# Performance work log

Hardware: AMD Instinct MI355X
Metric: run time of the kernel (lower is better)

## Reference

```python
import jax, jax.numpy as jnp
import numpy as np

B, L = 256, 8192
ACF_PAD = L - 1          # acf_class[1]
POOL = 8                 # acf_class[2]
ACF_SIZE = ACF_PAD + 1   # == L, length kept after trim
POOLED = ACF_SIZE // POOL  # 1024, MLP input size
LIN = [512, 256]
OUT = 4                  # no_reg=False -> 4 outputs


def _linear_init(key, fan_out, fan_in):
    kw, kb = jax.random.split(key)
    bound = 1.0 / np.sqrt(fan_in)
    W = jax.random.uniform(kw, (fan_out, fan_in), jnp.float32, -bound, bound)
    b = jax.random.uniform(kb, (fan_out,), jnp.float32, -bound, bound)
    return W, b


def setup_inputs() -> dict:
    key = jax.random.key(0)
    kx, k1, k2, k3 = jax.random.split(key, 4)
    x = jax.random.normal(kx, (B, 1, L), jnp.float32)
    W1, b1 = _linear_init(k1, LIN[0], POOLED)
    W2, b2 = _linear_init(k2, LIN[1], LIN[0])
    W3, b3 = _linear_init(k3, OUT, LIN[1])
    return {"x": x, "W1": W1, "b1": b1, "W2": W2, "b2": b2, "W3": W3, "b3": b3}


def reference(x, W1, b1, W2, b2, W3, b3):
    # x: [B, 1, L]. Grouped conv1d with groups=B == per-sample autocorrelation.
    a = x[:, 0, :]                                             # [B, L]
    # full cross-correlation of a with itself: [B, 2L-1], lags -(L-1)..(L-1)
    corr = jax.vmap(lambda v: jnp.correlate(v, v, mode="full"))(a)
    # trim [:, acf_pad:] keeps non-negative lags 0..L-1 -> length ACF_SIZE
    r = corr[:, L - 1:]                                        # [B, L]
    # MaxPool1d(POOL), stride == POOL, floor division (L divisible here)
    pooled = r.reshape(B, POOLED, POOL).max(axis=-1)           # [B, POOLED]
    # normalize by per-sample max
    norm = pooled / jnp.max(pooled, axis=1, keepdims=True)
    # MLP: (Dropout is identity at inference) Linear -> LeakyReLU x2 -> Linear
    h = jax.nn.leaky_relu(norm @ W1.T + b1, negative_slope=0.01)
    h = jax.nn.leaky_relu(h @ W2.T + b2, negative_slope=0.01)
    return h @ W3.T + b3                                       # [B, 4]
```

## Files before the change

### kernel.cpp

```cpp
#include <hip/hip_runtime.h>

typedef __attribute__((ext_vector_type(8))) short bf16x8;
typedef __attribute__((ext_vector_type(16))) float f32x16;

#define LN 8192
#define SA_ROWB 4240
#define SB_OFF  33920
#define SMEM_BYTES 65536

__device__ __forceinline__ unsigned short f2bf(float f) {
    unsigned int u = __float_as_uint(f);
    u += 0x7fffu + ((u >> 16) & 1u);
    return (unsigned short)(u >> 16);
}
__device__ __forceinline__ float lrelu(float v) { return v > 0.f ? v : 0.01f * v; }
__device__ __forceinline__ float gldx(const float* p, int i) { return (i >= 0 && i < LN) ? p[i] : 0.f; }

__device__ __forceinline__ void dot8bf(uint4 q, const float* nl, float& acc) {
    acc += __uint_as_float(q.x << 16)          * nl[0];
    acc += __uint_as_float(q.x & 0xffff0000u)  * nl[1];
    acc += __uint_as_float(q.y << 16)          * nl[2];
    acc += __uint_as_float(q.y & 0xffff0000u)  * nl[3];
    acc += __uint_as_float(q.z << 16)          * nl[4];
    acc += __uint_as_float(q.z & 0xffff0000u)  * nl[5];
    acc += __uint_as_float(q.w << 16)          * nl[6];
    acc += __uint_as_float(q.w & 0xffff0000u)  * nl[7];
}
__device__ __forceinline__ uint4 pack8(float4 a, float4 b) {
    uint4 pk;
    pk.x = (unsigned)f2bf(a.x) | ((unsigned)f2bf(a.y) << 16);
    pk.y = (unsigned)f2bf(a.z) | ((unsigned)f2bf(a.w) << 16);
    pk.z = (unsigned)f2bf(b.x) | ((unsigned)f2bf(b.y) << 16);
    pk.w = (unsigned)f2bf(b.z) | ((unsigned)f2bf(b.w) << 16);
    return pk;
}

__global__ __launch_bounds__(256)
void conv_kernel(const float* __restrict__ W1, const float* __restrict__ W2,
                 uint4* __restrict__ W1p, uint4* __restrict__ W2p)
{
    const int b = blockIdx.x, t = threadIdx.x;
    if (b < 256) {
        const int g = b * 256 + t;
        const int n = g >> 7, kqq = g & 127;
        const float4* src = (const float4*)(W1 + (size_t)n * 1024 + 8 * kqq);
        W1p[kqq * 512 + n] = pack8(src[0], src[1]);
    } else {
        const int g = (b - 256) * 256 + t;
        const int n = g >> 6, kqq = g & 63;
        const float4* src = (const float4*)(W2 + (size_t)n * 512 + 8 * kqq);
        W2p[kqq * 256 + n] = pack8(src[0], src[1]);
    }
}

__global__ __launch_bounds__(1024)
void fused_kernel(const float* __restrict__ x,
                  const uint4* __restrict__ W1p, const float* __restrict__ b1,
                  const uint4* __restrict__ W2p, const float* __restrict__ b2,
                  const float* __restrict__ W3, const float* __restrict__ b3,
                  float* __restrict__ out)
{
    __shared__ __align__(16) unsigned char smem[SMEM_BYTES];
    __shared__ float red[16];

    const int tid  = threadIdx.x;
    const int row  = blockIdx.x;
    const int lane = tid & 63;
    const int wv   = tid >> 6;
    const float* xr = x + (size_t)row * LN;

    const int jj = lane & 31;
    const int gp = lane >> 5;
    const int dd = lane & 7;
    const int hh = (lane >> 3) & 3;
    const int aoff_lane = dd * SA_ROWB + 64 + 16 * gp - 16 * hh;

    const int q  = wv & 3;
    const int p  = wv >> 2;
    const int T1 = p;
    const int T2 = 7 - p;
    const int s1 = 512 - 64 * p;
    const int s2 = 64 + 64 * p;

    for (int s = tid; s < 1156; s += 1024) {
        const int e0 = s * 8;
        float4 fa, fb;
        if (e0 + 7 < LN) {
            fa = *(const float4*)(xr + e0);
            fb = *(const float4*)(xr + e0 + 4);
        } else {
            fa = make_float4(gldx(xr,e0),   gldx(xr,e0+1), gldx(xr,e0+2), gldx(xr,e0+3));
            fb = make_float4(gldx(xr,e0+4), gldx(xr,e0+5), gldx(xr,e0+6), gldx(xr,e0+7));
        }
        uint4 pk = pack8(fa, fb);
        const int ph = s ^ ((s >> 3) & 7);
        *(uint4*)(smem + SB_OFF + ph * 16) = pk;
    }

    f32x16 acc1 = {}, acc2 = {};

    for (int ch = 0; ch < 4; ++ch) {
        const int tc = ch << 11;
        __syncthreads();
        if (tid < 528) {
            const int base = tc + 4 * tid - 40;
            float4 fa, fb, fc;
            if (base >= 0 && base + 11 < LN) {
                fa = *(const float4*)(xr + base);
                fb = *(const float4*)(xr + base + 4);
                fc = *(const float4*)(xr + base + 8);
            } else {
                fa = make_float4(gldx(xr,base),   gldx(xr,base+1), gldx(xr,base+2),  gldx(xr,base+3));
                fb = make_float4(gldx(xr,base+4), gldx(xr,base+5), gldx(xr,base+6),  gldx(xr,base+7));
                fc = make_float4(gldx(xr,base+8), gldx(xr,base+9), gldx(xr,base+10), gldx(xr,base+11));
            }
            unsigned short us[12];
            us[0]=f2bf(fa.x); us[1]=f2bf(fa.y); us[2]=f2bf(fa.z);  us[3]=f2bf(fa.w);
            us[4]=f2bf(fb.x); us[5]=f2bf(fb.y); us[6]=f2bf(fb.z);  us[7]=f2bf(fb.w);
            us[8]=f2bf(fc.x); us[9]=f2bf(fc.y); us[10]=f2bf(fc.z); us[11]=f2bf(fc.w);
            #pragma unroll
            for (int d = 0; d < 8; ++d) {
                unsigned long long pk = (unsigned long long)us[8-d]
                                      | ((unsigned long long)us[9-d]  << 16)
                                      | ((unsigned long long)us[10-d] << 32)
                                      | ((unsigned long long)us[11-d] << 48);
                *(unsigned long long*)(smem + d * SA_ROWB + 8 * tid) = pk;
            }
        }
        __syncthreads();

        const int c0 = ch * 128;
        int dD = s2 - c0; dD = dD < 0 ? 0 : (dD > 128 ? 128 : dD);
        int sLo = c0 > s2 ? c0 : s2;
        int sHi = (c0 + 128) < s1 ? (c0 + 128) : s1;
        int sS = sHi - sLo; if (sS < 0) sS = 0;
        const int wd0 = c0 + q * (dD >> 2),  wd1 = c0 + (q + 1) * (dD >> 2);
        const int ws0 = sLo + q * (sS >> 2), ws1 = sLo + (q + 1) * (sS >> 2);

        {
            const unsigned char* ap = smem + aoff_lane + 32 * (wd0 - c0);
            int S1 = 128 * T1 + 2 * wd0 + 4 * jj + gp;
            int S2 = 128 * T2 + 2 * wd0 + 4 * jj + gp;
            for (int mq = wd0; mq < wd1; mq += 4) {
                bf16x8 A[4], B1[4], B2[4];
                #pragma unroll
                for (int u = 0; u < 4; ++u) {
                    A[u] = *(const bf16x8*)(ap + 32 * u);
                    const int sa = S1 + 2 * u, sb = S2 + 2 * u;
                    B1[u] = *(const bf16x8*)(smem + SB_OFF + ((sa ^ ((sa >> 3) & 7)) << 4));
                    B2[u] = *(const bf16x8*)(smem + SB_OFF + ((sb ^ ((sb >> 3) & 7)) << 4));
                }
                #pragma unroll
                for (int u = 0; u < 4; ++u) {
                    acc1 = __builtin_amdgcn_mfma_f32_32x32x16_bf16(A[u], B1[u], acc1, 0, 0, 0);
                    acc2 = __builtin_amdgcn_mfma_f32_32x32x16_bf16(A[u], B2[u], acc2, 0, 0, 0);
                }
                ap += 128; S1 += 8; S2 += 8;
            }
        }
        {
            const unsigned char* ap = smem + aoff_lane + 32 * (ws0 - c0);
            int S1 = 128 * T1 + 2 * ws0 + 4 * jj + gp;
            for (int mq = ws0; mq < ws1; mq += 4) {
                bf16x8 A[4], B1[4];
                #pragma unroll
                for (int u = 0; u < 4; ++u) {
                    A[u] = *(const bf16x8*)(ap + 32 * u);
                    const int sa = S1 + 2 * u;
                    B1[u] = *(const bf16x8*)(smem + SB_OFF + ((sa ^ ((sa >> 3) & 7)) << 4));
                }
                #pragma unroll
                for (int u = 0; u < 4; ++u)
                    acc1 = __builtin_amdgcn_mfma_f32_32x32x16_bf16(A[u], B1[u], acc1, 0, 0, 0);
                ap += 128; S1 += 8;
            }
        }
    }

    __syncthreads();

    auto pwrite = [&](int T, int s, const f32x16& acc, bool add) {
        unsigned char* bp = smem + (T * 2 + s) * 4096 + jj * 128;
        #pragma unroll
        for (int rq = 0; rq < 4; ++rq) {
            const int bi = (2 * rq + gp) ^ (jj & 7);
            float4 w = make_float4(acc[4*rq], acc[4*rq+1], acc[4*rq+2], acc[4*rq+3]);
            float4* pp = (float4*)(bp + bi * 16);
            if (add) { float4 o = *pp; w.x += o.x; w.y += o.y; w.z += o.z; w.w += o.w; }
            *pp = w;
        }
    };
    if (q < 2) { pwrite(T1, q, acc1, false); pwrite(T2, q, acc2, false); }
    __syncthreads();
    if (q >= 2) { pwrite(T1, q - 2, acc1, true); pwrite(T2, q - 2, acc2, true); }
    __syncthreads();

    float* nrm = (float*)smem;
    float* h1  = (float*)(smem + 4096);
    float* h2  = (float*)(smem + 6144);
    float* ph  = (float*)(smem + 7168);
    float* pe  = (float*)(smem + 9216);

    {
        const int T  = tid >> 7;
        const int j2 = (tid >> 2) & 31;
        const int rq = tid & 3;
        const unsigned char* b0 = smem + (T * 2) * 4096 + j2 * 128;
        const int biA = (2 * rq)     ^ (j2 & 7);
        const int biB = (2 * rq + 1) ^ (j2 & 7);
        float4 s0a = *(const float4*)(b0 + biA * 16);
        float4 s0b = *(const float4*)(b0 + biB * 16);
        float4 s1a = *(const float4*)(b0 + 4096 + biA * 16);
        float4 s1b = *(const float4*)(b0 + 4096 + biB * 16);
        float v0 = s0a.x + s1a.x, v1 = s0a.y + s1a.y, v2 = s0a.z + s1a.z, v3 = s0a.w + s1a.w;
        float v4 = s0b.x + s1b.x, v5 = s0b.y + s1b.y, v6 = s0b.z + s1b.z, v7 = s0b.w + s1b.w;
        float m = fmaxf(fmaxf(fmaxf(v0, v1), fmaxf(v2, v3)), fmaxf(fmaxf(v4, v5), fmaxf(v6, v7)));

        float mx = m;
        for (int off = 32; off > 0; off >>= 1) mx = fmaxf(mx, __shfl_xor(mx, off));
        if (lane == 0) red[wv] = mx;
        __syncthreads();
        float pmax = red[0];
        #pragma unroll
        for (int k = 1; k < 16; ++k) pmax = fmaxf(pmax, red[k]);
        nrm[tid] = m * (1.0f / pmax);
    }
    __syncthreads();

    {
        const int n  = tid & 511;
        const int kh = tid >> 9;
        const float4* n4 = (const float4*)nrm;
        const uint4* wp = W1p + (size_t)kh * 64 * 512 + n;
        float acc = 0.f;
        #pragma unroll 8
        for (int kq = 0; kq < 64; ++kq) {
            uint4 qw = wp[kq * 512];
            float4 a = n4[kh * 128 + 2 * kq];
            float4 b = n4[kh * 128 + 2 * kq + 1];
            float nl[8] = {a.x, a.y, a.z, a.w, b.x, b.y, b.z, b.w};
            dot8bf(qw, nl, acc);
        }
        if (kh == 1) ph[n] = acc;
        __syncthreads();
        if (kh == 0) h1[n] = lrelu(acc + ph[n] + b1[n]);
    }
    __syncthreads();

    {
        const int n  = tid & 255;
        const int qd = tid >> 8;
        const float4* h4 = (const float4*)h1;
        const uint4* wp = W2p + (size_t)qd * 16 * 256 + n;
        float acc = 0.f;
        #pragma unroll
        for (int kq = 0; kq < 16; ++kq) {
            uint4 qw = wp[kq * 256];
            float4 a = h4[qd * 32 + 2 * kq];
            float4 b = h4[qd * 32 + 2 * kq + 1];
            float nl[8] = {a.x, a.y, a.z, a.w, b.x, b.y, b.z, b.w};
            dot8bf(qw, nl, acc);
        }
        if (qd > 0) pe[(qd - 1) * 256 + n] = acc;
        __syncthreads();
        if (qd == 0) h2[n] = lrelu(acc + pe[n] + pe[256 + n] + pe[512 + n] + b2[n]);
    }
    __syncthreads();

    if (wv < 4) {
        const float4 w = ((const float4*)(W3 + wv * 256))[lane];
        const float4 a = ((const float4*)h2)[lane];
        float s = w.x*a.x + w.y*a.y + w.z*a.z + w.w*a.w;
        for (int off = 32; off > 0; off >>= 1) s += __shfl_xor(s, off);
        if (lane == 0) out[row * 4 + wv] = s + b3[wv];
    }
}

extern "C" void kernel_launch(void* const* d_in, const int* in_sizes, int n_in,
                              void* d_out, int out_size, void* d_ws, size_t ws_size,
                              hipStream_t stream)
{
    const float* x  = (const float*)d_in[0];
    const float* W1 = (const float*)d_in[1];
    const float* b1 = (const float*)d_in[2];
    const float* W2 = (const float*)d_in[3];
    const float* b2 = (const float*)d_in[4];
    const float* W3 = (const float*)d_in[5];
    const float* b3 = (const float*)d_in[6];
    float* outp = (float*)d_out;
    uint4* W1p = (uint4*)d_ws;
    uint4* W2p = (uint4*)((char*)d_ws + (1 << 20));

    hipLaunchKernelGGL(conv_kernel,  dim3(320), dim3(256),  0, stream, W1, W2, W1p, W2p);
    hipLaunchKernelGGL(fused_kernel, dim3(256), dim3(1024), 0, stream,
                       x, W1p, b1, W2p, b2, W3, b3, outp);
}
```

Before: 45.48 us.

## Repartition MFMA work so each wave reuses A fragments across four output tiles

```diff
diff --git a/kernel.cpp b/kernel.cpp
--- a/kernel.cpp
+++ b/kernel.cpp
@@ -75,12 +75,8 @@
     const int hh = (lane >> 3) & 3;
     const int aoff_lane = dd * SA_ROWB + 64 + 16 * gp - 16 * hh;
 
-    const int q  = wv & 3;
-    const int p  = wv >> 2;
-    const int T1 = p;
-    const int T2 = 7 - p;
-    const int s1 = 512 - 64 * p;
-    const int s2 = 64 + 64 * p;
+    const int g = wv & 1;
+    const int w = wv >> 1;
 
     for (int s = tid; s < 1156; s += 1024) {
         const int e0 = s * 8;
@@ -97,7 +93,7 @@
         *(uint4*)(smem + SB_OFF + ph * 16) = pk;
     }
 
-    f32x16 acc1 = {}, acc2 = {};
+    f32x16 a0 = {}, a1 = {}, a2 = {}, a3 = {};
 
     for (int ch = 0; ch < 4; ++ch) {
         const int tc = ch << 11;
@@ -130,49 +126,47 @@
         __syncthreads();
 
         const int c0 = ch * 128;
-        int dD = s2 - c0; dD = dD < 0 ? 0 : (dD > 128 ? 128 : dD);
-        int sLo = c0 > s2 ? c0 : s2;
-        int sHi = (c0 + 128) < s1 ? (c0 + 128) : s1;
-        int sS = sHi - sLo; if (sS < 0) sS = 0;
-        const int wd0 = c0 + q * (dD >> 2),  wd1 = c0 + (q + 1) * (dD >> 2);
-        const int ws0 = sLo + q * (sS >> 2), ws1 = sLo + (q + 1) * (sS >> 2);
-
-        {
-            const unsigned char* ap = smem + aoff_lane + 32 * (wd0 - c0);
-            int S1 = 128 * T1 + 2 * wd0 + 4 * jj + gp;
-            int S2 = 128 * T2 + 2 * wd0 + 4 * jj + gp;
-            for (int mq = wd0; mq < wd1; mq += 4) {
-                bf16x8 A[4], B1[4], B2[4];
-                #pragma unroll
-                for (int u = 0; u < 4; ++u) {
-                    A[u] = *(const bf16x8*)(ap + 32 * u);
-                    const int sa = S1 + 2 * u, sb = S2 + 2 * u;
-                    B1[u] = *(const bf16x8*)(smem + SB_OFF + ((sa ^ ((sa >> 3) & 7)) << 4));
-                    B2[u] = *(const bf16x8*)(smem + SB_OFF + ((sb ^ ((sb >> 3) & 7)) << 4));
+        int r0a, r1a, nta, r0b, r1b, ntb;
+        if (g == 0) {
+            r0a = c0 + 16 * w; r1a = r0a + 16; nta = 4 - ch;
+            r0b = 0; r1b = 0; ntb = 0;
+        } else {
+            r0a = c0 + 8 * w;      r1a = r0a + 8; nta = 4 - ch;
+            r0b = c0 + 64 + 8 * w; r1b = r0b + 8; ntb = 3 - ch;
+            if (ntb <= 0) { r1b = r0b; ntb = 0; }
+        }
+
+        #pragma unroll
+        for (int rg = 0; rg < 2; ++rg) {
+            const int m0 = rg ? r0b : r0a;
+            const int m1 = rg ? r1b : r1a;
+            const int nt = rg ? ntb : nta;
+            const unsigned char* ap = smem + aoff_lane + 32 * (m0 - c0);
+            int Sb = 128 * g + 2 * m0 + 4 * jj + gp;
+            #pragma unroll 2
+            for (int mq = m0; mq < m1; ++mq) {
+                bf16x8 A = *(const bf16x8*)ap;
+                {
+                    const int s = Sb;
+                    bf16x8 B = *(const bf16x8*)(smem + SB_OFF + ((s ^ ((s >> 3) & 7)) << 4));
+                    a0 = __builtin_amdgcn_mfma_f32_32x32x16_bf16(A, B, a0, 0, 0, 0);
                 }
-                #pragma unroll
-                for (int u = 0; u < 4; ++u) {
-                    acc1 = __builtin_amdgcn_mfma_f32_32x32x16_bf16(A[u], B1[u], acc1, 0, 0, 0);
-                    acc2 = __builtin_amdgcn_mfma_f32_32x32x16_bf16(A[u], B2[u], acc2, 0, 0, 0);
+                if (nt > 1) {
+                    const int s = Sb + 256;
+                    bf16x8 B = *(const bf16x8*)(smem + SB_OFF + ((s ^ ((s >> 3) & 7)) << 4));
+                    a1 = __builtin_amdgcn_mfma_f32_32x32x16_bf16(A, B, a1, 0, 0, 0);
                 }
-                ap += 128; S1 += 8; S2 += 8;
-            }
-        }
-        {
-            const unsigned char* ap = smem + aoff_lane + 32 * (ws0 - c0);
-            int S1 = 128 * T1 + 2 * ws0 + 4 * jj + gp;
-            for (int mq = ws0; mq < ws1; mq += 4) {
-                bf16x8 A[4], B1[4];
-                #pragma unroll
-                for (int u = 0; u < 4; ++u) {
-                    A[u] = *(const bf16x8*)(ap + 32 * u);
-                    const int sa = S1 + 2 * u;
-                    B1[u] = *(const bf16x8*)(smem + SB_OFF + ((sa ^ ((sa >> 3) & 7)) << 4));
+                if (nt > 2) {
+                    const int s = Sb + 512;
+                    bf16x8 B = *(const bf16x8*)(smem + SB_OFF + ((s ^ ((s >> 3) & 7)) << 4));
+                    a2 = __builtin_amdgcn_mfma_f32_32x32x16_bf16(A, B, a2, 0, 0, 0);
                 }
-                #pragma unroll
-                for (int u = 0; u < 4; ++u)
-                    acc1 = __builtin_amdgcn_mfma_f32_32x32x16_bf16(A[u], B1[u], acc1, 0, 0, 0);
-                ap += 128; S1 += 8;
+                if (nt > 3) {
+                    const int s = Sb + 768;
+                    bf16x8 B = *(const bf16x8*)(smem + SB_OFF + ((s ^ ((s >> 3) & 7)) << 4));
+                    a3 = __builtin_amdgcn_mfma_f32_32x32x16_bf16(A, B, a3, 0, 0, 0);
+                }
+                ap += 32; Sb += 2;
             }
         }
     }
@@ -184,16 +178,27 @@
         #pragma unroll
         for (int rq = 0; rq < 4; ++rq) {
             const int bi = (2 * rq + gp) ^ (jj & 7);
-            float4 w = make_float4(acc[4*rq], acc[4*rq+1], acc[4*rq+2], acc[4*rq+3]);
+            float4 wt = make_float4(acc[4*rq], acc[4*rq+1], acc[4*rq+2], acc[4*rq+3]);
             float4* pp = (float4*)(bp + bi * 16);
-            if (add) { float4 o = *pp; w.x += o.x; w.y += o.y; w.z += o.z; w.w += o.w; }
-            *pp = w;
+            if (add) { float4 o = *pp; wt.x += o.x; wt.y += o.y; wt.z += o.z; wt.w += o.w; }
+            *pp = wt;
         }
     };
-    if (q < 2) { pwrite(T1, q, acc1, false); pwrite(T2, q, acc2, false); }
-    __syncthreads();
-    if (q >= 2) { pwrite(T1, q - 2, acc1, true); pwrite(T2, q - 2, acc2, true); }
-    __syncthreads();
+    {
+        const int slot  = w & 1;
+        const int phase = w >> 1;
+        #pragma unroll
+        for (int pi = 0; pi < 4; ++pi) {
+            if (phase == pi) {
+                const bool add = (pi > 0);
+                pwrite(g,     slot, a0, add);
+                pwrite(g + 2, slot, a1, add);
+                pwrite(g + 4, slot, a2, add);
+                pwrite(g + 6, slot, a3, add);
+            }
+            __syncthreads();
+        }
+    }
 
     float* nrm = (float*)smem;
     float* h1  = (float*)(smem + 4096);
@@ -268,9 +273,9 @@
     __syncthreads();
 
     if (wv < 4) {
-        const float4 w = ((const float4*)(W3 + wv * 256))[lane];
+        const float4 wt = ((const float4*)(W3 + wv * 256))[lane];
         const float4 a = ((const float4*)h2)[lane];
-        float s = w.x*a.x + w.y*a.y + w.z*a.z + w.w*a.w;
+        float s = wt.x*a.x + wt.y*a.y + wt.z*a.z + wt.w*a.w;
         for (int off = 32; off > 0; off >>= 1) s += __shfl_xor(s, off);
         if (lane == 0) out[row * 4 + wv] = s + b3[wv];
     }
```

Result: slower. 55.06 us (+21.1%).
